# Kernel tuning notes

Hardware: AMD Instinct MI355X
Metric: run time of the kernel (lower is better)

The kernel has to match this reference:

```python
import jax, jax.numpy as jnp
import numpy as np

B, C, H, W = 4, 3, 256, 256
L, WIDTH, M1, M2 = 4, 32, 12, 12


def setup_inputs() -> dict:
    key = jax.random.key(0)
    ks = jax.random.split(key, 13)
    scale = 1.0 / (WIDTH * WIDTH)
    return {
        "x": jax.random.uniform(ks[0], (B, C, H, W), jnp.float32),
        "p_w": jax.random.normal(ks[1], (C + 2, WIDTH), jnp.float32) * 0.3,
        "p_b": jax.random.normal(ks[2], (WIDTH,), jnp.float32) * 0.1,
        "sw1r": scale * jax.random.uniform(ks[3], (L, WIDTH, WIDTH, M1, M2), jnp.float32),
        "sw1i": scale * jax.random.uniform(ks[4], (L, WIDTH, WIDTH, M1, M2), jnp.float32),
        "sw2r": scale * jax.random.uniform(ks[5], (L, WIDTH, WIDTH, M1, M2), jnp.float32),
        "sw2i": scale * jax.random.uniform(ks[6], (L, WIDTH, WIDTH, M1, M2), jnp.float32),
        "cw": jax.random.normal(ks[7], (L, WIDTH, WIDTH), jnp.float32) * 0.15,
        "cb": jax.random.normal(ks[8], (L, WIDTH), jnp.float32) * 0.1,
        "mlp0_w": jax.random.normal(ks[9], (WIDTH, 128), jnp.float32) * 0.15,
        "mlp0_b": jax.random.normal(ks[10], (128,), jnp.float32) * 0.1,
        "mlp1_w": jax.random.normal(ks[11], (128, C), jnp.float32) * 0.1,
        "mlp1_b": jax.random.normal(ks[12], (C,), jnp.float32) * 0.1,
    }


def _spectral_conv(h, w1, w2):
    # h: (B, Cin, H, W); w1/w2: (Cin, Cout, M1, M2) complex
    b, ci, hh, ww = h.shape
    hf = jnp.fft.rfft2(h)  # (B, Cin, H, W//2+1)
    out_ft = jnp.zeros((b, w1.shape[1], hf.shape[2], hf.shape[3]), jnp.complex64)
    out_ft = out_ft.at[:, :, :M1, :M2].set(
        jnp.einsum('bixy,ioxy->boxy', hf[:, :, :M1, :M2], w1))
    out_ft = out_ft.at[:, :, -M1:, :M2].set(
        jnp.einsum('bixy,ioxy->boxy', hf[:, :, -M1:, :M2], w2))
    return jnp.fft.irfft2(out_ft, s=(hh, ww))


def reference(x, p_w, p_b, sw1r, sw1i, sw2r, sw2i, cw, cb, mlp0_w, mlp0_b, mlp1_w, mlp1_b):
    b, c, hh, ww = x.shape
    gx = jnp.broadcast_to(jnp.linspace(0.0, 1.0, hh)[None, :, None, None], (b, hh, ww, 1))
    gy = jnp.broadcast_to(jnp.linspace(0.0, 1.0, ww)[None, None, :, None], (b, hh, ww, 1))
    feat = jnp.concatenate([x.transpose(0, 2, 3, 1), gx, gy], axis=-1)  # (B,H,W,C+2)
    h = (feat @ p_w + p_b).transpose(0, 3, 1, 2)  # (B, width, H, W)
    for l in range(L):
        w1 = sw1r[l] + 1j * sw1i[l]
        w2 = sw2r[l] + 1j * sw2i[l]
        bypass = jnp.einsum('bihw,io->bohw', h, cw[l]) + cb[l][None, :, None, None]
        h2 = _spectral_conv(h, w1, w2) + bypass
        h = jax.nn.gelu(h2, approximate=False) if l < L - 1 else h2
    h = h.transpose(0, 2, 3, 1)  # (B,H,W,width)
    h = jax.nn.gelu(h @ mlp0_w + mlp0_b, approximate=False)
    out = h @ mlp1_w + mlp1_b
    return out.transpose(0, 3, 1, 2)  # (B, out_channels, H, W)
```

## Files before the change

### kernel.cpp

```cpp
#include <hip/hip_runtime.h>
#include <math.h>


#define ANG0 0.024543692606170260f
#define H_STRIDE 65600

typedef __attribute__((ext_vector_type(8))) short bf16x8_t;
typedef __attribute__((ext_vector_type(4))) float f32x4_t;

__device__ __forceinline__ float fgelu(float v) {
    float u = v * 0.70710678118f;
    float a = fabsf(u);
    float t = __builtin_amdgcn_rcpf(__builtin_fmaf(0.3275911f, a, 1.0f));
    float p = t * __builtin_fmaf(t, __builtin_fmaf(t, __builtin_fmaf(t,
                  __builtin_fmaf(t, 1.061405429f, -1.453152027f),
                  1.421413741f), -0.284496736f), 0.254829592f);
    float e = __expf(-u * u);
    float er = __builtin_fmaf(-p, e, 1.0f);
    er = copysignf(er, u);
    return 0.5f * v * (1.0f + er);
}

__device__ __forceinline__ unsigned packsplit(float v) {
    unsigned u = __float_as_uint(v);
    unsigned hi = u & 0xffff0000u;
    float r = v - __uint_as_float(hi);
    return hi | (__float_as_uint(r) >> 16);
}

__device__ __forceinline__ void fill_csp(float2* sCSP, int tid, int nthr) {
    for (int p = tid; p < 256; p += nthr)
        sCSP[p] = make_float2(cosf(p * ANG0), sinf(p * ANG0));
}

__device__ __forceinline__ void ky_dft_tail(const float* sVp, const float2* sCSP,
                                            float* tmp, int b, int x, int y) {
    for (int idx = y; idx < 384; idx += 256) {
        int o = idx / 12, ky = idx % 12;
        const float* vp = sVp + o * 258;
        float vdc = vp[0], v128 = vp[256];
        float aR0 = vdc + ((ky & 1) ? -v128 : v128);
        float aR1 = 0.f, aI0 = 0.f, aI1 = 0.f;
#pragma unroll 4
        for (int yy = 1; yy <= 126; yy += 2) {
            int p0 = (ky * yy) & 255;
            int p1 = (p0 + ky) & 255;
            float2 c0 = sCSP[p0], c1 = sCSP[p1];
            float2 v0 = *reinterpret_cast<const float2*>(vp + 2 * yy);
            float2 v1 = *reinterpret_cast<const float2*>(vp + 2 * (yy + 1));
            aR0 = __builtin_fmaf(v0.x + v0.y, c0.x, aR0);
            aI0 = __builtin_fmaf(v0.x - v0.y, -c0.y, aI0);
            aR1 = __builtin_fmaf(v1.x + v1.y, c1.x, aR1);
            aI1 = __builtin_fmaf(v1.x - v1.y, -c1.y, aI1);
        }
        {
            int p = (ky * 127) & 255;
            float2 c = sCSP[p];
            float2 v0 = *reinterpret_cast<const float2*>(vp + 254);
            aR0 = __builtin_fmaf(v0.x + v0.y, c.x, aR0);
            aI0 = __builtin_fmaf(v0.x - v0.y, -c.y, aI0);
        }
        reinterpret_cast<float2*>(tmp + (((size_t)(b * 32 + o)) * 256 + x) * 24)[ky] =
            make_float2(aR0 + aR1, aI0 + aI1);
    }
}

__device__ __forceinline__ float c2val(int y, int j) {
    if (j >= 24 || j == 1) return 0.f;
    if (j == 0) return 1.f;
    int q = j >> 1;
    float ang = ((q * y) & 255) * ANG0;
    return (j & 1) ? -2.f * sinf(ang) : 2.f * cosf(ang);
}
__device__ __forceinline__ float etval(int j, int y) {
    if (j >= 24) return 0.f;
    int q = j >> 1;
    float ang = ((q * y) & 255) * ANG0;
    return (j & 1) ? -sinf(ang) : cosf(ang);
}
__device__ __forceinline__ void pack2(unsigned* dsthi, unsigned* dstlo,
                                      float v0, float v1) {
    unsigned u0 = __float_as_uint(v0), u1 = __float_as_uint(v1);
    *dsthi = ((u1 >> 16) << 16) | (u0 >> 16);
    float r0 = v0 - __uint_as_float(u0 & 0xffff0000u);
    float r1 = v1 - __uint_as_float(u1 & 0xffff0000u);
    *dstlo = ((__float_as_uint(r1) >> 16) << 16) | (__float_as_uint(r0) >> 16);
}

__global__ void k_init(const float* __restrict__ w0, const float* __restrict__ b0,
                       const float* __restrict__ w1, const float* __restrict__ cw,
                       unsigned* __restrict__ specA, unsigned* __restrict__ tailA,
                       unsigned* __restrict__ cwB, unsigned* __restrict__ wB,
                       float* __restrict__ w1p) {
    int t = threadIdx.x;
    const float SC = 1.0f / 65536.0f;
    for (int idx = t; idx < 4096; idx += 256) {
        int w = idx & 3, lane = (idx >> 2) & 63, mt = idx >> 8;
        int y = mt * 16 + (lane & 15);
        int j0 = 8 * (lane >> 4) + 2 * w;
        pack2(&specA[idx], &specA[4096 + idx],
              c2val(y, j0) * SC, c2val(y, j0 + 1) * SC);
    }
    for (int idx = t; idx < 4096; idx += 256) {
        int w = idx & 3, lane = (idx >> 2) & 63, tt = idx >> 8;
        int kk = tt >> 1, mtj = tt & 1;
        int j = mtj * 16 + (lane & 15);
        int y0 = kk * 32 + 8 * (lane >> 4) + 2 * w;
        pack2(&tailA[idx], &tailA[4096 + idx], etval(j, y0), etval(j, y0 + 1));
    }
    for (int idx = t; idx < 2048; idx += 256) {
        int w = idx & 3, lane = (idx >> 2) & 63, tt = idx >> 8;
        int l = tt >> 1, n = tt & 1;
        int o = n * 16 + (lane & 15);
        int i0 = 8 * (lane >> 4) + 2 * w;
        pack2(&cwB[idx], &cwB[2048 + idx],
              cw[l * 1024 + i0 * 32 + o], cw[l * 1024 + (i0 + 1) * 32 + o]);
    }
    for (int idx = t; idx < 2048; idx += 256) {
        int jw = idx & 3, lane = (idx >> 2) & 63, n = idx >> 8;
        int i0 = 8 * (lane >> 4) + 2 * jw;
        int km = n * 16 + (lane & 15);
        pack2(&wB[idx], &wB[2048 + idx], w0[i0 * 128 + km], w0[(i0 + 1) * 128 + km]);
    }
    for (int idx = t; idx < 384; idx += 256) {
        int c = idx >> 7, km = idx & 127;
        w1p[idx] = w1[km * 3 + c];
    }
}

__global__ __launch_bounds__(256, 4) void k_liftf(const float* __restrict__ xin,
                                                  const float* __restrict__ pw,
                                                  const float* __restrict__ pb,
                                                  unsigned* __restrict__ h,
                                                  float* __restrict__ tmp) {
    __shared__ float sVp[32 * 258];
    __shared__ float2 sCSP[256];
    int b = blockIdx.x >> 8, x = blockIdx.x & 255, y = threadIdx.x;
    fill_csp(sCSP, y, 256);
    int vslot = 2 * ((y <= 128) ? y : 256 - y) + ((y > 128) ? 1 : 0);
    float f0 = xin[((b * 3 + 0) * 256 + x) * 256 + y];
    float f1 = xin[((b * 3 + 1) * 256 + x) * 256 + y];
    float f2 = xin[((b * 3 + 2) * 256 + x) * 256 + y];
    float gx = x * (1.0f / 255.0f), gy = y * (1.0f / 255.0f);
#pragma unroll
    for (int o = 0; o < 32; ++o) {
        float v = pb[o] + f0 * pw[o] + f1 * pw[32 + o] + f2 * pw[64 + o]
                + gx * pw[96 + o] + gy * pw[128 + o];
        h[(size_t)(b * 32 + o) * H_STRIDE + x * 256 + y] = packsplit(v);
        sVp[o * 258 + vslot] = v;
    }
    __syncthreads();
    ky_dft_tail(sVp, sCSP, tmp, b, x, y);
}

__global__ __launch_bounds__(320) void k_dftx(const float* __restrict__ tmp,
                                              float* __restrict__ hfp) {
    __shared__ float sT[1536];
    __shared__ float2 sCSP[256];
    int plane = blockIdx.x >> 2, part = blockIdx.x & 3;
    int x0 = part * 64;
    int tid = threadIdx.x;
    fill_csp(sCSP, tid, 320);
    for (int idx = tid; idx < 1536; idx += 320)
        sT[idx] = tmp[(size_t)plane * 6144 + x0 * 24 + idx];
    __syncthreads();
    if (tid < 288) {
        int kxi = tid / 12, ky = tid % 12;
        int kxv = kxi < 12 ? kxi : 232 + kxi;
        float aR = 0.f, aI = 0.f;
        for (int xp = 0; xp < 64; ++xp) {
            int p = (kxv * (x0 + xp)) & 255;
            float2 cs2 = sCSP[p];
            float tr = sT[xp * 24 + 2 * ky], ti = sT[xp * 24 + 2 * ky + 1];
            aR += tr * cs2.x + ti * cs2.y;
            aI += ti * cs2.x - tr * cs2.y;
        }
        hfp[(((size_t)part * 128 + plane) * 24 + kxi) * 24 + 2 * ky]     = aR;
        hfp[(((size_t)part * 128 + plane) * 24 + kxi) * 24 + 2 * ky + 1] = aI;
    }
}

__global__ __launch_bounds__(320) void k_mixcinv(const float* __restrict__ hfp,
                                                 const float* __restrict__ w1r,
                                                 const float* __restrict__ w1i,
                                                 const float* __restrict__ w2r,
                                                 const float* __restrict__ w2i,
                                                 float* __restrict__ g, int l) {
    __shared__ float sA[576];
    __shared__ float2 sCSP[256];
    int b = blockIdx.x >> 5, o = blockIdx.x & 31;
    int tid = threadIdx.x;
    fill_csp(sCSP, tid, 320);
    if (tid < 288) {
        int kxi = tid / 12, ky = tid % 12;
        const float *wr, *wi;
        int rk;
        if (kxi < 12) { wr = w1r; wi = w1i; rk = kxi; }
        else          { wr = w2r; wi = w2i; rk = kxi - 12; }
        size_t wbase = ((size_t)l * 32 * 32) * 144 + (size_t)o * 144 + rk * 12 + ky;
        size_t hbase = (((size_t)(b * 32)) * 24 + kxi) * 24 + 2 * ky;
        float aR = 0.f, aI = 0.f;
#pragma unroll 4
        for (int i = 0; i < 32; ++i) {
            float2 h0 = *reinterpret_cast<const float2*>(hfp + hbase + i * 576);
            float2 h1 = *reinterpret_cast<const float2*>(hfp + 73728 + hbase + i * 576);
            float2 h2 = *reinterpret_cast<const float2*>(hfp + 147456 + hbase + i * 576);
            float2 h3 = *reinterpret_cast<const float2*>(hfp + 221184 + hbase + i * 576);
            float hr = h0.x + h1.x + h2.x + h3.x;
            float hi = h0.y + h1.y + h2.y + h3.y;
            float wrv = wr[wbase + (size_t)i * 4608];
            float wiv = wi[wbase + (size_t)i * 4608];
            aR += hr * wrv - hi * wiv;
            aI += hr * wiv + hi * wrv;
        }
        sA[kxi * 24 + 2 * ky]     = aR;
        sA[kxi * 24 + 2 * ky + 1] = aI;
    }
    __syncthreads();
    if (tid < 256) {
        int x = tid;
        float out[24];
#pragma unroll
        for (int j = 0; j < 24; ++j) out[j] = 0.f;
        for (int kxi = 0; kxi < 24; ++kxi) {
            int kxv = kxi < 12 ? kxi : 232 + kxi;
            int p = (kxv * x) & 255;
            float2 cs2 = sCSP[p];
#pragma unroll
            for (int ky = 0; ky < 12; ++ky) {
                float ar = sA[kxi * 24 + 2 * ky], ai = sA[kxi * 24 + 2 * ky + 1];
                out[2 * ky]     += ar * cs2.x - ai * cs2.y;
                out[2 * ky + 1] += ar * cs2.y + ai * cs2.x;
            }
        }
        float* gp = g + ((size_t)(b * 32 + o)) * 6144 + x * 24;
#pragma unroll
        for (int j = 0; j < 24; ++j) gp[j] = out[j];
    }
}

template <int ACT, int WRITEH>
__device__ __forceinline__ void dinv_phaseA(const unsigned* __restrict__ hU,
                                            unsigned* __restrict__ hW,
                                            const float* __restrict__ g,
                                            const unsigned* __restrict__ specA,
                                            const unsigned* __restrict__ cwB,
                                            const float* __restrict__ cb,
                                            unsigned* sVvT, int b, int x, int l,
                                            int wv, int lane) {
    int l15 = lane & 15, l4 = lane >> 4;
    unsigned hbuf[4][8];
    {
        const unsigned* hp = hU + (size_t)(b * 32) * H_STRIDE + x * 256;
#pragma unroll
        for (int mtl = 0; mtl < 4; ++mtl) {
            int mtg = wv * 4 + mtl;
#pragma unroll
            for (int j = 0; j < 8; ++j)
                hbuf[mtl][j] = hp[(size_t)(8 * l4 + j) * H_STRIDE + mtg * 16 + l15];
        }
    }
    bf16x8_t Ghi[2], Glo[2];
#pragma unroll
    for (int n = 0; n < 2; ++n) {
        float gv[8];
        if (l4 < 3) {
            const float* gp = g + (size_t)(b * 32 + n * 16 + l15) * 6144
                            + x * 24 + 8 * l4;
            float4 a = *reinterpret_cast<const float4*>(gp);
            float4 c = *reinterpret_cast<const float4*>(gp + 4);
            gv[0] = a.x; gv[1] = a.y; gv[2] = a.z; gv[3] = a.w;
            gv[4] = c.x; gv[5] = c.y; gv[6] = c.z; gv[7] = c.w;
        } else {
#pragma unroll
            for (int j = 0; j < 8; ++j) gv[j] = 0.f;
        }
#pragma unroll
        for (int j = 0; j < 8; ++j) {
            float v = gv[j];
            unsigned u = __float_as_uint(v);
            Ghi[n][j] = (short)(u >> 16);
            float r = v - __uint_as_float(u & 0xffff0000u);
            Glo[n][j] = (short)(__float_as_uint(r) >> 16);
        }
    }
    bf16x8_t Whi[2], Wlo[2];
#pragma unroll
    for (int n = 0; n < 2; ++n) {
        Whi[n] = *reinterpret_cast<const bf16x8_t*>(cwB + ((l * 2 + n) * 64 + lane) * 4);
        Wlo[n] = *reinterpret_cast<const bf16x8_t*>(cwB + 2048 + ((l * 2 + n) * 64 + lane) * 4);
    }
    float cbb[2] = {cb[l * 32 + l15], cb[l * 32 + 16 + l15]};
#pragma unroll
    for (int mtl = 0; mtl < 4; ++mtl) {
        int mtg = wv * 4 + mtl;
        bf16x8_t C2hi = *reinterpret_cast<const bf16x8_t*>(specA + (mtg * 64 + lane) * 4);
        bf16x8_t C2lo = *reinterpret_cast<const bf16x8_t*>(specA + 4096 + (mtg * 64 + lane) * 4);
        bf16x8_t Hhi, Hlo;
#pragma unroll
        for (int j = 0; j < 8; ++j) {
            unsigned u = hbuf[mtl][j];
            Hhi[j] = (short)(u >> 16);
            Hlo[j] = (short)(u & 0xffffu);
        }
#pragma unroll
        for (int n = 0; n < 2; ++n) {
            f32x4_t acc = {0.f, 0.f, 0.f, 0.f};
            acc = __builtin_amdgcn_mfma_f32_16x16x32_bf16(C2hi, Ghi[n], acc, 0, 0, 0);
            acc = __builtin_amdgcn_mfma_f32_16x16x32_bf16(C2lo, Ghi[n], acc, 0, 0, 0);
            acc = __builtin_amdgcn_mfma_f32_16x16x32_bf16(C2hi, Glo[n], acc, 0, 0, 0);
            acc = __builtin_amdgcn_mfma_f32_16x16x32_bf16(Hhi, Whi[n], acc, 0, 0, 0);
            acc = __builtin_amdgcn_mfma_f32_16x16x32_bf16(Hlo, Whi[n], acc, 0, 0, 0);
            acc = __builtin_amdgcn_mfma_f32_16x16x32_bf16(Hhi, Wlo[n], acc, 0, 0, 0);
            uint4 pu;
            {
                float v0 = acc[0] + cbb[n], v1 = acc[1] + cbb[n];
                float v2 = acc[2] + cbb[n], v3 = acc[3] + cbb[n];
                if (ACT) { v0 = fgelu(v0); v1 = fgelu(v1); v2 = fgelu(v2); v3 = fgelu(v3); }
                pu.x = packsplit(v0); pu.y = packsplit(v1);
                pu.z = packsplit(v2); pu.w = packsplit(v3);
            }
            *reinterpret_cast<uint4*>(&sVvT[(n * 16 + l15) * 260 + mtg * 16 + l4 * 4]) = pu;
            if (WRITEH)
                *reinterpret_cast<uint4*>(hW + (size_t)(b * 32 + n * 16 + l15) * H_STRIDE
                                          + x * 256 + mtg * 16 + l4 * 4) = pu;
        }
    }
}

__global__ __launch_bounds__(256) void k_dinvf(unsigned* __restrict__ h,
                                               const float* __restrict__ g,
                                               const unsigned* __restrict__ specA,
                                               const unsigned* __restrict__ tailA,
                                               const unsigned* __restrict__ cwB,
                                               const float* __restrict__ cb,
                                               float* __restrict__ tmp, int l) {
    __shared__ unsigned sVvT[32 * 260];
    int b = blockIdx.x >> 8, x = blockIdx.x & 255;
    int tid = threadIdx.x, wv = tid >> 6, lane = tid & 63;
    int l15 = lane & 15, l4 = lane >> 4;
    dinv_phaseA<1, 1>(h, h, g, specA, cwB, cb, sVvT, b, x, l, wv, lane);
    __syncthreads();
    {
        int mtj = wv >> 1, nq = wv & 1;
        f32x4_t acc = {0.f, 0.f, 0.f, 0.f};
        for (int kk = 0; kk < 8; ++kk) {
            bf16x8_t Ehi = *reinterpret_cast<const bf16x8_t*>(
                tailA + ((kk * 2 + mtj) * 64 + lane) * 4);
            bf16x8_t Elo = *reinterpret_cast<const bf16x8_t*>(
                tailA + 4096 + ((kk * 2 + mtj) * 64 + lane) * 4);
            int base = (nq * 16 + l15) * 260 + kk * 32 + 8 * l4;
            uint4 va = *reinterpret_cast<const uint4*>(&sVvT[base]);
            uint4 vb = *reinterpret_cast<const uint4*>(&sVvT[base + 4]);
            bf16x8_t Vhi, Vlo;
            Vhi[0] = (short)(va.x >> 16); Vlo[0] = (short)(va.x & 0xffffu);
            Vhi[1] = (short)(va.y >> 16); Vlo[1] = (short)(va.y & 0xffffu);
            Vhi[2] = (short)(va.z >> 16); Vlo[2] = (short)(va.z & 0xffffu);
            Vhi[3] = (short)(va.w >> 16); Vlo[3] = (short)(va.w & 0xffffu);
            Vhi[4] = (short)(vb.x >> 16); Vlo[4] = (short)(vb.x & 0xffffu);
            Vhi[5] = (short)(vb.y >> 16); Vlo[5] = (short)(vb.y & 0xffffu);
            Vhi[6] = (short)(vb.z >> 16); Vlo[6] = (short)(vb.z & 0xffffu);
            Vhi[7] = (short)(vb.w >> 16); Vlo[7] = (short)(vb.w & 0xffffu);
            acc = __builtin_amdgcn_mfma_f32_16x16x32_bf16(Ehi, Vhi, acc, 0, 0, 0);
            acc = __builtin_amdgcn_mfma_f32_16x16x32_bf16(Ehi, Vlo, acc, 0, 0, 0);
            acc = __builtin_amdgcn_mfma_f32_16x16x32_bf16(Elo, Vhi, acc, 0, 0, 0);
        }
        int j0 = mtj * 16 + l4 * 4;
        if (j0 < 24) {
            float4 st = {acc[0], acc[1], acc[2], acc[3]};
            *reinterpret_cast<float4*>(
                tmp + (size_t)(b * 32 + nq * 16 + l15) * 6144 + x * 24 + j0) = st;
        }
    }
}

__global__ __launch_bounds__(256) void k_dinvmlp(const unsigned* __restrict__ h,
                                                 const float* __restrict__ g,
                                                 const unsigned* __restrict__ specA,
                                                 const unsigned* __restrict__ cwB,
                                                 const float* __restrict__ cb,
                                                 const unsigned* __restrict__ wB,
                                                 const float* __restrict__ b0,
                                                 const float* __restrict__ w1p,
                                                 const float* __restrict__ b1,
                                                 float* __restrict__ out) {
    __shared__ unsigned sVvT[32 * 260];
    __shared__ float sOut[256 * 5];
    int b = blockIdx.x >> 8, x = blockIdx.x & 255;
    int tid = threadIdx.x, wv = tid >> 6, lane = tid & 63;
    int l15 = lane & 15, l4 = lane >> 4;
    dinv_phaseA<0, 0>(h, nullptr, g, specA, cwB, cb, sVvT, b, x, 3, wv, lane);
    __syncthreads();
    bf16x8_t Ahi[4], Alo[4];
#pragma unroll
    for (int mt = 0; mt < 4; ++mt) {
        int rowY = (wv << 6) + (mt << 4) + l15;
#pragma unroll
        for (int j = 0; j < 8; ++j) {
            unsigned u = sVvT[(8 * l4 + j) * 260 + rowY];
            Ahi[mt][j] = (short)(u >> 16);
            Alo[mt][j] = (short)(u & 0xffffu);
        }
    }
    float apart[4][4][3];
#pragma unroll
    for (int mt = 0; mt < 4; ++mt)
#pragma unroll
        for (int r = 0; r < 4; ++r)
#pragma unroll
            for (int c = 0; c < 3; ++c) apart[mt][r][c] = 0.f;
    for (int n = 0; n < 8; ++n) {
        bf16x8_t Bhi = *reinterpret_cast<const bf16x8_t*>(wB + (n * 64 + lane) * 4);
        bf16x8_t Blo = *reinterpret_cast<const bf16x8_t*>(wB + 2048 + (n * 64 + lane) * 4);
        int km = (n << 4) + l15;
        float b0v  = b0[km];
        float w1v0 = w1p[km], w1v1 = w1p[128 + km], w1v2 = w1p[256 + km];
#pragma unroll
        for (int mt = 0; mt < 4; ++mt) {
            f32x4_t acc = {0.f, 0.f, 0.f, 0.f};
            acc = __builtin_amdgcn_mfma_f32_16x16x32_bf16(Ahi[mt], Bhi, acc, 0, 0, 0);
            acc = __builtin_amdgcn_mfma_f32_16x16x32_bf16(Ahi[mt], Blo, acc, 0, 0, 0);
            acc = __builtin_amdgcn_mfma_f32_16x16x32_bf16(Alo[mt], Bhi, acc, 0, 0, 0);
#pragma unroll
            for (int r = 0; r < 4; ++r) {
                float tg = fgelu(acc[r] + b0v);
                apart[mt][r][0] = __builtin_fmaf(tg, w1v0, apart[mt][r][0]);
                apart[mt][r][1] = __builtin_fmaf(tg, w1v1, apart[mt][r][1]);
                apart[mt][r][2] = __builtin_fmaf(tg, w1v2, apart[mt][r][2]);
            }
        }
    }
#pragma unroll
    for (int mt = 0; mt < 4; ++mt)
#pragma unroll
        for (int r = 0; r < 4; ++r)
#pragma unroll
            for (int c = 0; c < 3; ++c) {
                float v = apart[mt][r][c];
                v += __shfl_xor(v, 1);
                v += __shfl_xor(v, 2);
                v += __shfl_xor(v, 4);
                v += __shfl_xor(v, 8);
                if (l15 == 0)
                    sOut[((wv << 6) + (mt << 4) + (l4 << 2) + r) * 5 + c] = v;
            }
    __syncthreads();
    float b1v0 = b1[0], b1v1 = b1[1], b1v2 = b1[2];
    out[(((size_t)b * 3 + 0) * 256 + x) * 256 + tid] = sOut[tid * 5 + 0] + b1v0;
    out[(((size_t)b * 3 + 1) * 256 + x) * 256 + tid] = sOut[tid * 5 + 1] + b1v1;
    out[(((size_t)b * 3 + 2) * 256 + x) * 256 + tid] = sOut[tid * 5 + 2] + b1v2;
}

extern "C" void kernel_launch(void* const* d_in, const int* in_sizes, int n_in,
                              void* d_out, int out_size, void* d_ws, size_t ws_size,
                              hipStream_t stream) {
    const float* xin  = (const float*)d_in[0];
    const float* pw   = (const float*)d_in[1];
    const float* pb   = (const float*)d_in[2];
    const float* sw1r = (const float*)d_in[3];
    const float* sw1i = (const float*)d_in[4];
    const float* sw2r = (const float*)d_in[5];
    const float* sw2i = (const float*)d_in[6];
    const float* cw   = (const float*)d_in[7];
    const float* cb   = (const float*)d_in[8];
    const float* w0   = (const float*)d_in[9];
    const float* b0   = (const float*)d_in[10];
    const float* w1   = (const float*)d_in[11];
    const float* b1   = (const float*)d_in[12];
    float* out = (float*)d_out;

    unsigned* specA = (unsigned*)d_ws;
    unsigned* tailA = specA + 8192;
    unsigned* cwB   = tailA + 8192;
    unsigned* wB    = cwB + 4096;
    float* w1p = (float*)(wB + 4096);
    unsigned* h = (unsigned*)(w1p + 384);
    float* tmp = (float*)(h + (size_t)128 * H_STRIDE);
    float* hfp = tmp + 786432;
    float* g   = tmp;

    k_init<<<1, 256, 0, stream>>>(w0, b0, w1, cw, specA, tailA, cwB, wB, w1p);
    k_liftf<<<1024, 256, 0, stream>>>(xin, pw, pb, h, tmp);
    for (int l = 0; l < 4; ++l) {
        k_dftx<<<512, 320, 0, stream>>>(tmp, hfp);
        k_mixcinv<<<128, 320, 0, stream>>>(hfp, sw1r, sw1i, sw2r, sw2i, g, l);
        if (l < 3)
            k_dinvf<<<1024, 256, 0, stream>>>(h, g, specA, tailA, cwB, cb, tmp, l);
        else
            k_dinvmlp<<<1024, 256, 0, stream>>>(h, g, specA, cwB, cb, wB, b0, w1p,
                                                b1, out);
    }
}
```

Measured before the change: 218.8 us.

## Split final inverse-DFT+MLP kernel into single-wave blocks over 32-column y slices

The last-layer kernel now launches 8192 single-wavefront blocks, each handling 32 y positions of one (b,x) row, instead of 1024 blocks of 256 threads. It inlines its own phase-A computation (inverse spectral MFMA plus the 1x1 bypass conv) in place of the shared dinv_phaseA helper, and uses a much smaller shared-memory tile. The goal is more parallelism and occupancy, with less shared memory and register pressure per block. In exchange, the per-block loads of g, the weights and the MLP weights are repeated across 8x more blocks.

```diff
diff --git a/kernel.cpp b/kernel.cpp
--- a/kernel.cpp
+++ b/kernel.cpp
@@ -374,37 +374,108 @@
     }
 }
 
-__global__ __launch_bounds__(256) void k_dinvmlp(const unsigned* __restrict__ h,
-                                                 const float* __restrict__ g,
-                                                 const unsigned* __restrict__ specA,
-                                                 const unsigned* __restrict__ cwB,
-                                                 const float* __restrict__ cb,
-                                                 const unsigned* __restrict__ wB,
-                                                 const float* __restrict__ b0,
-                                                 const float* __restrict__ w1p,
-                                                 const float* __restrict__ b1,
-                                                 float* __restrict__ out) {
-    __shared__ unsigned sVvT[32 * 260];
-    __shared__ float sOut[256 * 5];
-    int b = blockIdx.x >> 8, x = blockIdx.x & 255;
-    int tid = threadIdx.x, wv = tid >> 6, lane = tid & 63;
+__global__ __launch_bounds__(64) void k_dinvmlp(const unsigned* __restrict__ h,
+                                                const float* __restrict__ g,
+                                                const unsigned* __restrict__ specA,
+                                                const unsigned* __restrict__ cwB,
+                                                const float* __restrict__ cb,
+                                                const unsigned* __restrict__ wB,
+                                                const float* __restrict__ b0,
+                                                const float* __restrict__ w1p,
+                                                const float* __restrict__ b1,
+                                                float* __restrict__ out) {
+    __shared__ unsigned sV[32 * 36];
+    __shared__ float sOut[32 * 5];
+    int bid = blockIdx.x;
+    int b = bid >> 11, x = (bid >> 3) & 255, ys = bid & 7;
+    int lane = threadIdx.x;
     int l15 = lane & 15, l4 = lane >> 4;
-    dinv_phaseA<0, 0>(h, nullptr, g, specA, cwB, cb, sVvT, b, x, 3, wv, lane);
+    unsigned hbuf[2][8];
+    {
+        const unsigned* hp = h + (size_t)(b * 32) * H_STRIDE + x * 256;
+#pragma unroll
+        for (int mtl = 0; mtl < 2; ++mtl) {
+            int mtg = ys * 2 + mtl;
+#pragma unroll
+            for (int j = 0; j < 8; ++j)
+                hbuf[mtl][j] = hp[(size_t)(8 * l4 + j) * H_STRIDE + mtg * 16 + l15];
+        }
+    }
+    bf16x8_t Ghi[2], Glo[2];
+#pragma unroll
+    for (int n = 0; n < 2; ++n) {
+        float gv[8];
+        if (l4 < 3) {
+            const float* gp = g + (size_t)(b * 32 + n * 16 + l15) * 6144
+                            + x * 24 + 8 * l4;
+            float4 a = *reinterpret_cast<const float4*>(gp);
+            float4 c = *reinterpret_cast<const float4*>(gp + 4);
+            gv[0] = a.x; gv[1] = a.y; gv[2] = a.z; gv[3] = a.w;
+            gv[4] = c.x; gv[5] = c.y; gv[6] = c.z; gv[7] = c.w;
+        } else {
+#pragma unroll
+            for (int j = 0; j < 8; ++j) gv[j] = 0.f;
+        }
+#pragma unroll
+        for (int j = 0; j < 8; ++j) {
+            float v = gv[j];
+            unsigned u = __float_as_uint(v);
+            Ghi[n][j] = (short)(u >> 16);
+            float r = v - __uint_as_float(u & 0xffff0000u);
+            Glo[n][j] = (short)(__float_as_uint(r) >> 16);
+        }
+    }
+    bf16x8_t Whi[2], Wlo[2];
+#pragma unroll
+    for (int n = 0; n < 2; ++n) {
+        Whi[n] = *reinterpret_cast<const bf16x8_t*>(cwB + ((6 + n) * 64 + lane) * 4);
+        Wlo[n] = *reinterpret_cast<const bf16x8_t*>(cwB + 2048 + ((6 + n) * 64 + lane) * 4);
+    }
+    float cbb[2] = {cb[96 + l15], cb[96 + 16 + l15]};
+#pragma unroll
+    for (int mtl = 0; mtl < 2; ++mtl) {
+        int mtg = ys * 2 + mtl;
+        bf16x8_t C2hi = *reinterpret_cast<const bf16x8_t*>(specA + (mtg * 64 + lane) * 4);
+        bf16x8_t C2lo = *reinterpret_cast<const bf16x8_t*>(specA + 4096 + (mtg * 64 + lane) * 4);
+        bf16x8_t Hhi, Hlo;
+#pragma unroll
+        for (int j = 0; j < 8; ++j) {
+            unsigned u = hbuf[mtl][j];
+            Hhi[j] = (short)(u >> 16);
+            Hlo[j] = (short)(u & 0xffffu);
+        }
+#pragma unroll
+        for (int n = 0; n < 2; ++n) {
+            f32x4_t acc = {0.f, 0.f, 0.f, 0.f};
+            acc = __builtin_amdgcn_mfma_f32_16x16x32_bf16(C2hi, Ghi[n], acc, 0, 0, 0);
+            acc = __builtin_amdgcn_mfma_f32_16x16x32_bf16(C2lo, Ghi[n], acc, 0, 0, 0);
+            acc = __builtin_amdgcn_mfma_f32_16x16x32_bf16(C2hi, Glo[n], acc, 0, 0, 0);
+            acc = __builtin_amdgcn_mfma_f32_16x16x32_bf16(Hhi, Whi[n], acc, 0, 0, 0);
+            acc = __builtin_amdgcn_mfma_f32_16x16x32_bf16(Hlo, Whi[n], acc, 0, 0, 0);
+            acc = __builtin_amdgcn_mfma_f32_16x16x32_bf16(Hhi, Wlo[n], acc, 0, 0, 0);
+            uint4 pu;
+            pu.x = packsplit(acc[0] + cbb[n]);
+            pu.y = packsplit(acc[1] + cbb[n]);
+            pu.z = packsplit(acc[2] + cbb[n]);
+            pu.w = packsplit(acc[3] + cbb[n]);
+            *reinterpret_cast<uint4*>(&sV[(n * 16 + l15) * 36 + mtl * 16 + l4 * 4]) = pu;
+        }
+    }
     __syncthreads();
-    bf16x8_t Ahi[4], Alo[4];
-#pragma unroll
-    for (int mt = 0; mt < 4; ++mt) {
-        int rowY = (wv << 6) + (mt << 4) + l15;
+    bf16x8_t Ahi[2], Alo[2];
+#pragma unroll
+    for (int mt = 0; mt < 2; ++mt) {
+        int rowY = mt * 16 + l15;
 #pragma unroll
         for (int j = 0; j < 8; ++j) {
-            unsigned u = sVvT[(8 * l4 + j) * 260 + rowY];
+            unsigned u = sV[(8 * l4 + j) * 36 + rowY];
             Ahi[mt][j] = (short)(u >> 16);
             Alo[mt][j] = (short)(u & 0xffffu);
         }
     }
-    float apart[4][4][3];
-#pragma unroll
-    for (int mt = 0; mt < 4; ++mt)
+    float apart[2][4][3];
+#pragma unroll
+    for (int mt = 0; mt < 2; ++mt)
 #pragma unroll
         for (int r = 0; r < 4; ++r)
 #pragma unroll
@@ -416,7 +487,7 @@
         float b0v  = b0[km];
         float w1v0 = w1p[km], w1v1 = w1p[128 + km], w1v2 = w1p[256 + km];
 #pragma unroll
-        for (int mt = 0; mt < 4; ++mt) {
+        for (int mt = 0; mt < 2; ++mt) {
             f32x4_t acc = {0.f, 0.f, 0.f, 0.f};
             acc = __builtin_amdgcn_mfma_f32_16x16x32_bf16(Ahi[mt], Bhi, acc, 0, 0, 0);
             acc = __builtin_amdgcn_mfma_f32_16x16x32_bf16(Ahi[mt], Blo, acc, 0, 0, 0);
@@ -431,7 +502,7 @@
         }
     }
 #pragma unroll
-    for (int mt = 0; mt < 4; ++mt)
+    for (int mt = 0; mt < 2; ++mt)
 #pragma unroll
         for (int r = 0; r < 4; ++r)
 #pragma unroll
@@ -442,13 +513,15 @@
                 v += __shfl_xor(v, 4);
                 v += __shfl_xor(v, 8);
                 if (l15 == 0)
-                    sOut[((wv << 6) + (mt << 4) + (l4 << 2) + r) * 5 + c] = v;
+                    sOut[(mt * 16 + (l4 << 2) + r) * 5 + c] = v;
             }
     __syncthreads();
-    float b1v0 = b1[0], b1v1 = b1[1], b1v2 = b1[2];
-    out[(((size_t)b * 3 + 0) * 256 + x) * 256 + tid] = sOut[tid * 5 + 0] + b1v0;
-    out[(((size_t)b * 3 + 1) * 256 + x) * 256 + tid] = sOut[tid * 5 + 1] + b1v1;
-    out[(((size_t)b * 3 + 2) * 256 + x) * 256 + tid] = sOut[tid * 5 + 2] + b1v2;
+    if (lane < 32) {
+        int y = ys * 32 + lane;
+        out[(((size_t)b * 3 + 0) * 256 + x) * 256 + y] = sOut[lane * 5 + 0] + b1[0];
+        out[(((size_t)b * 3 + 1) * 256 + x) * 256 + y] = sOut[lane * 5 + 1] + b1[1];
+        out[(((size_t)b * 3 + 2) * 256 + x) * 256 + y] = sOut[lane * 5 + 2] + b1[2];
+    }
 }
 
 extern "C" void kernel_launch(void* const* d_in, const int* in_sizes, int n_in,
@@ -487,7 +560,7 @@
         if (l < 3)
             k_dinvf<<<1024, 256, 0, stream>>>(h, g, specA, tailA, cwB, cb, tmp, l);
         else
-            k_dinvmlp<<<1024, 256, 0, stream>>>(h, g, specA, cwB, cb, wB, b0, w1p,
-                                                b1, out);
-    }
-}
+            k_dinvmlp<<<8192, 64, 0, stream>>>(h, g, specA, cwB, cb, wB, b0, w1p,
+                                               b1, out);
+    }
+}
```

After: 218.4 us. About the same (-0.2%).
